# Optimization experiments

Measured on AMD Instinct MI355X. Metric: run time of the kernel, lower is better.

Reference implementation:

```python
import jax, jax.numpy as jnp
import numpy as np

N_SAMPLES = 32768
WINDOW = 512
STEP = WINDOW // 2            # 256
N_FRAMES = N_SAMPLES // STEP  # 128
N_COEFFS = WINDOW // 2 + 1    # 257
CPD = 16
N_RES = 32
EXPR = 4
BASE_RES = 0.5
CTRL_FRAMES = N_SAMPLES // 256  # 128 control frames, step=256


def fft_convolve(a, b):
    # zero-pad to 2N, multiply spectra, keep first N samples (matching repo's fft_convolve)
    n = max(a.shape[-1], b.shape[-1])
    fa = jnp.fft.rfft(a, n=2 * n, axis=-1)
    fb = jnp.fft.rfft(b, n=2 * n, axis=-1)
    out = jnp.fft.irfft(fa * fb, n=2 * n, axis=-1)
    return out[..., :n]


def upsample_with_holes(x, n_samples):
    # insert zeros between samples: out[..., ::step] = x
    lead, frames = x.shape[:-1], x.shape[-1]
    step = n_samples // frames
    out = jnp.zeros(lead + (frames, step), x.dtype)
    out = out.at[..., 0].set(x)
    return out.reshape(lead + (n_samples,))


def interpolate_last_axis(x, out_size):
    # linear interpolation along last axis (F.interpolate mode='linear', align_corners=False)
    in_size = x.shape[-1]
    scale = in_size / out_size
    pos = (jnp.arange(out_size, dtype=x.dtype) + 0.5) * scale - 0.5
    pos = jnp.clip(pos, 0.0, in_size - 1)
    lo = jnp.floor(pos).astype(jnp.int32)
    hi = jnp.minimum(lo + 1, in_size - 1)
    w = (pos - lo.astype(x.dtype))
    return x[..., lo] * (1.0 - w) + x[..., hi] * w


def materialize_resonances(amp, phase, decay):
    # amp/phase/decay: (R, C, E) -> (R, E, C)
    amp = jnp.transpose(amp, (0, 2, 1))
    phase = jnp.transpose(phase, (0, 2, 1))
    decay = jnp.transpose(decay, (0, 2, 1))
    d = BASE_RES + jax.nn.sigmoid(decay) * (1.0 - BASE_RES) * 0.9   # per-frame decay in (0.5, 0.95)
    start_phase = jnp.tanh(phase) * np.pi
    start_mags = jnp.abs(amp)
    # log-space scan of exponentially decaying spectral magnitudes: mags[t] = start * d^(t+1)
    t = jnp.arange(1, N_FRAMES + 1, dtype=amp.dtype)                  # (T,)
    log_mags = jnp.log(start_mags + 1e-12)[..., None, :] + t[:, None] * jnp.log(d)[..., None, :]
    spec = jnp.exp(log_mags) * jnp.exp(1j * start_phase[..., None, :])  # (R,E,T,C)
    frames = jnp.fft.irfft(spec, n=WINDOW, axis=-1)                     # (R,E,T,W)
    # overlap-add with hop STEP (W = 2*STEP): split halves, scatter into (T+1) slots
    first, second = frames[..., :STEP], frames[..., STEP:]
    out = jnp.zeros(frames.shape[:-2] + (N_FRAMES + 1, STEP), frames.dtype)
    out = out.at[..., :N_FRAMES, :].add(first)
    out = out.at[..., 1:, :].add(second)
    out = out.reshape(frames.shape[:-2] + ((N_FRAMES + 1) * STEP,))[..., :N_SAMPLES]
    return out.reshape(1, 1, N_RES, EXPR, N_SAMPLES)


def setup_inputs() -> dict:
    key = jax.random.key(0)
    ks = jax.random.split(key, 8)
    control_signal = jax.random.normal(ks[0], (2, 4, CPD, CTRL_FRAMES), dtype=jnp.float32)
    deformations = jax.random.normal(ks[1], (2, 4, EXPR, CTRL_FRAMES), dtype=jnp.float32)
    router = jax.random.uniform(ks[2], (CPD, N_RES), minval=-1.0, maxval=1.0, dtype=jnp.float32)
    gains = jax.random.uniform(ks[3], (N_RES, 1), minval=0.01, maxval=1.1, dtype=jnp.float32)
    amp = jax.random.uniform(ks[4], (N_RES, N_COEFFS, EXPR), minval=0.01, maxval=1.0, dtype=jnp.float32)
    phase = jax.random.uniform(ks[5], (N_RES, N_COEFFS, EXPR), minval=0.01, maxval=1.0, dtype=jnp.float32)
    decay = jax.random.uniform(ks[6], (N_RES, N_COEFFS, EXPR), minval=0.01, maxval=1.0, dtype=jnp.float32)
    impulse_noise = jax.random.uniform(ks[7], (128,), minval=-1.0, maxval=1.0, dtype=jnp.float32)
    return dict(control_signal=control_signal, deformations=deformations, router=router,
                gains=gains, amp=amp, phase=phase, decay=decay, impulse_noise=impulse_noise)


def reference(control_signal, deformations, router, gains, amp, phase, decay, impulse_noise):
    res = materialize_resonances(amp, phase, decay)            # (1,1,R,E,S)
    res = res / (jnp.linalg.norm(res, axis=-1, keepdims=True) + 1e-8)  # unit_norm

    B, NE, C, F = control_signal.shape
    routed = jnp.einsum('bncf,cr->bnrf', control_signal, router)  # (B,NE,R,F)
    before_upsample = routed

    routed = upsample_with_holes(routed[:, :, :, None, :], N_SAMPLES)  # (B,NE,R,1,S)

    n = jnp.arange(128, dtype=jnp.float32)
    hamming = 0.54 - 0.46 * jnp.cos(2.0 * jnp.pi * n / 128.0)  # torch periodic hamming
    impulse = hamming * impulse_noise
    impulse = jnp.pad(impulse, (0, N_SAMPLES - 128)).reshape(1, 1, 1, 1, N_SAMPLES)

    routed = fft_convolve(impulse, routed)
    conv = fft_convolve(routed, res)                           # (B,NE,R,E,S)

    base = jnp.zeros_like(deformations).at[:, :, 0:1, :].set(1.0)
    d = jax.nn.softmax(base + deformations, axis=-2)           # (B,NE,E,F)
    d = interpolate_last_axis(d[:, :, None, :, :], N_SAMPLES)  # (B,NE,1,E,S)

    x = jnp.sum(d * conv, axis=-2)                             # (B,NE,R,S)
    summed = jnp.tanh(x * jnp.abs(gains).reshape(1, 1, N_RES, 1))
    summed = jnp.sum(summed, axis=-2, keepdims=True)           # (B,NE,1,S)
    return summed, before_upsample
```

## Files before the change

kernel.cpp:

```cpp
#include <hip/hip_runtime.h>
#include <hip/hip_bf16.h>
#include <math.h>

#define N_SAMPLES 32768
#define STEP 256
#define N_FRAMES 128
#define N_COEFFS 257
#define KT 576
#define NKS 18
#define CPD 16
#define N_RES 32
#define EXPR 4
#define CTRL 128
#define NBN 8
#define BSTR 40
#define PI_F 3.14159265358979323846f

typedef __attribute__((ext_vector_type(8))) short bf16x8;
typedef __attribute__((ext_vector_type(4))) float f32x4;

__device__ __forceinline__ unsigned short f2bf(float x) {
    __hip_bfloat16 h = __float2bfloat16(x);
    return *(unsigned short*)&h;
}

__device__ __forceinline__ float bf2f(short u) {
    return __bfloat162float(*(__hip_bfloat16*)&u);
}

__device__ __forceinline__ float ftanh(float x) {
    float e = exp2f(x * 2.885390081777927f);
    return 1.0f - 2.0f * __builtin_amdgcn_rcpf(e + 1.0f);
}

__global__ __launch_bounds__(256) void k1m(const float* __restrict__ amp,
                                           const float* __restrict__ phase,
                                           const float* __restrict__ decay,
                                           float* __restrict__ res_raw,
                                           float* __restrict__ normp,
                                           float* __restrict__ out_zero) {
    __shared__ __align__(16) short Bs[2][64 * BSTR];
    __shared__ __align__(16) short Pb[KT];
    __shared__ __align__(16) short Zb[KT];
    __shared__ __align__(16) float Lf[KT];
    __shared__ __align__(16) float costab[512];
    __shared__ float red[256];
    int tid = threadIdx.x;
    int l = tid & 63, w = tid >> 6;
    int bid = blockIdx.x;
    out_zero[(size_t)bid * 256 + tid] = 0.f;
    int x = bid & 7, m = bid >> 3;
    int re = x * 16 + (m >> 3);
    int sub = m & 7;
    int bx = sub >> 1, jb = sub & 1;
    int r = re >> 2, e = re & 3;

    for (int i = tid; i < 512; i += 256)
        costab[i] = cosf((float)i * (2.0f * PI_F / 512.0f));

    for (int k = tid; k < KT; k += 256) {
        int kk = (k < 288) ? k : k - 288;
        float P = 0.f, Z = 0.f, L2v = 0.f;
        if (kk < N_COEFFS) {
            int src = (r * N_COEFFS + kk) * EXPR + e;
            float mm = fabsf(amp[src]) + 1e-12f;
            float ph = tanhf(phase[src]) * PI_F;
            float sg = 1.0f / (1.0f + expf(-decay[src]));
            float d  = 0.5f + 0.45f * sg;
            float wk = (kk == 0 || kk == 256) ? (1.0f / 512.0f) : (2.0f / 512.0f);
            float c  = (k < 288) ? (wk * mm * cosf(ph)) : (-wk * mm * sinf(ph));
            float sgn = (kk & 1) ? -1.f : 1.f;
            P = c * (d + sgn);
            Z = c * d;
            L2v = log2f(d);
        }
        int kloc = k & 31, blk = k >> 5;
        int p = blk * 32 + ((kloc >> 2) & 3) * 8 + ((kloc >> 4) & 1) * 4 + (kloc & 3);
        Pb[p] = (short)f2bf(P);
        Zb[p] = (short)f2bf(Z);
        Lf[p] = L2v;
    }
    __syncthreads();

    int o = (bx * 4 + w) * 16 + (l & 15);
    int g4v = l >> 4;
    float cb[8], sb[8], cc[8], sc[8];
    #pragma unroll
    for (int ee = 0; ee < 8; ++ee) {
        int delta = ((ee >> 2) << 4) + (g4v << 2) + (ee & 3);
        int xx = (delta * o) & 511;
        cb[ee] = costab[xx];
        sb[ee] = costab[(xx + 384) & 511];
        cc[ee] = cb[ee]; sc[ee] = sb[ee];
    }
    float rc, rs;
    {
        int xr = (32 * o) & 511;
        rc = costab[xr];
        rs = costab[(xr + 384) & 511];
    }

    int gj = tid >> 2;
    int gg = tid & 3;
    int jf = jb * 64 + gj;
    float jf_f = (float)jf;

    f32x4 acc[4] = {{0.f,0.f,0.f,0.f},{0.f,0.f,0.f,0.f},{0.f,0.f,0.f,0.f},{0.f,0.f,0.f,0.f}};
    int rrow = l & 15;
    int rcol = (l >> 4) * 8;

    auto GEN = [&](int s, int buf) {
        int kbp = s * 32 + gg * 8;
        bf16x8 vv;
        if (jf == 0) {
            vv = *(const bf16x8*)&Zb[kbp];
        } else {
            bf16x8 Pp = *(const bf16x8*)&Pb[kbp];
            f32x4 l0 = *(const f32x4*)&Lf[kbp];
            f32x4 l1 = *(const f32x4*)&Lf[kbp + 4];
            #pragma unroll
            for (int q = 0; q < 4; ++q) {
                vv[q]     = (short)f2bf(bf2f(Pp[q])     * exp2f(jf_f * l0[q]));
                vv[4 + q] = (short)f2bf(bf2f(Pp[4 + q]) * exp2f(jf_f * l1[q]));
            }
        }
        *(bf16x8*)&Bs[buf][gj * BSTR + gg * 8] = vv;
    };

    GEN(0, 0);
    __syncthreads();
    #pragma unroll
    for (int s = 0; s < NKS; ++s) {
        if (s < NKS - 1) GEN(s + 1, (s + 1) & 1);
        if (s == 9) {
            #pragma unroll
            for (int ee = 0; ee < 8; ++ee) { cc[ee] = cb[ee]; sc[ee] = sb[ee]; }
        }
        bf16x8 af;
        #pragma unroll
        for (int ee = 0; ee < 8; ++ee)
            af[ee] = (short)f2bf((s < 9) ? cc[ee] : sc[ee]);
        if (s != 8 && s != NKS - 1) {
            #pragma unroll
            for (int ee = 0; ee < 8; ++ee) {
                float t = cc[ee] * rc - sc[ee] * rs;
                sc[ee] = fmaf(cc[ee], rs, sc[ee] * rc);
                cc[ee] = t;
            }
        }
        const short* bp = &Bs[s & 1][0];
        #pragma unroll
        for (int jt = 0; jt < 4; ++jt) {
            bf16x8 bf = *(const bf16x8*)(bp + (jt * 16 + rrow) * BSTR + rcol);
            acc[jt] = __builtin_amdgcn_mfma_f32_16x16x32_bf16(af, bf, acc[jt], 0, 0, 0);
        }
        __syncthreads();
    }

    int otile = bx * 4 + w;
    int o0 = otile * 16 + ((l >> 4) & 3) * 4;
    int jbase = jb * 64 + (l & 15);
    float s2 = 0.f;
    #pragma unroll
    for (int jt = 0; jt < 4; ++jt) {
        int j = jbase + jt * 16;
        float4 v = make_float4(acc[jt][0], acc[jt][1], acc[jt][2], acc[jt][3]);
        s2 += v.x * v.x + v.y * v.y + v.z * v.z + v.w * v.w;
        *(float4*)&res_raw[(size_t)re * N_SAMPLES + j * STEP + o0] = v;
    }
    red[tid] = s2;
    __syncthreads();
    for (int st = 128; st > 0; st >>= 1) {
        if (tid < st) red[tid] += red[tid + st];
        __syncthreads();
    }
    if (tid == 0) normp[re * 8 + bx * 2 + jb] = red[0];
}

__global__ __launch_bounds__(256) void k3_impconv(const float* __restrict__ res_raw,
                                                  const float* __restrict__ normp,
                                                  const float* __restrict__ noise,
                                                  const float* __restrict__ control,
                                                  const float* __restrict__ router,
                                                  float* __restrict__ out_w,
                                                  uint4* __restrict__ Gbf_q) {
    __shared__ __align__(16) float st[8320];
    __shared__ __align__(16) float imp[128];
    int bid = blockIdx.x;
    int tid = threadIdx.x;
    if (bid >= 512) {
        int idx = (bid - 512) * 256 + tid;
        int f  = idx % CTRL;
        int r  = (idx / CTRL) % N_RES;
        int bn = idx / (CTRL * N_RES);
        float s = 0.f;
        #pragma unroll
        for (int c = 0; c < CPD; ++c)
            s += control[(bn * CPD + c) * CTRL + f] * router[c * N_RES + r];
        out_w[idx] = s;
        return;
    }
    int r  = (bid & 7) * 4 + ((bid >> 3) & 3);
    int t2 = bid >> 5;
    int e  = t2 & 3;
    int kt = t2 >> 2;
    int re = r * 4 + e;
    float ns = 0.f;
    #pragma unroll
    for (int i = 0; i < 8; ++i) ns += normp[re * 8 + i];
    float inv = 1.0f / (sqrtf(ns) + 1e-8f);
    if (tid < 128)
        imp[tid] = (0.54f - 0.46f * cosf((2.0f * PI_F / 128.0f) * (float)tid)) * noise[tid];
    const float* rp = res_raw + (size_t)re * N_SAMPLES;
    int gbase = kt * 8192 - 127;
    for (int i = tid; i < 8320; i += 256) {
        int g = gbase + i;
        st[i] = (g >= 0 && g < N_SAMPLES) ? rp[g] * inv : 0.f;
    }
    __syncthreads();

    int jg = tid >> 6;
    int o0 = (tid & 63) * 4;
    int jl[8];
    #pragma unroll
    for (int hh = 0; hh < 4; ++hh) {
        int h = jg * 4 + hh;
        int j0 = ((h >> 1) & 1) * 16 + (h >> 2) * 4 + (h & 1) * 2;
        jl[2 * hh] = j0;
        jl[2 * hh + 1] = j0 + 1;
    }
    float4 cur[8];
    float acc[8][4] = {};
    #pragma unroll
    for (int w = 0; w < 8; ++w)
        cur[w] = *(const float4*)&st[jl[w] * 256 + o0];

    for (int v = 0; v < 128; v += 4) {
        float4 im = *(const float4*)&imp[124 - v];
        float wt[4] = {im.w, im.z, im.y, im.x};
        #pragma unroll
        for (int w = 0; w < 8; ++w) {
            float4 nx = *(const float4*)&st[jl[w] * 256 + o0 + v + 4];
            float win[8] = {cur[w].x, cur[w].y, cur[w].z, cur[w].w, nx.x, nx.y, nx.z, nx.w};
            #pragma unroll
            for (int k = 0; k < 4; ++k)
                #pragma unroll
                for (int d = 0; d < 4; ++d)
                    acc[w][d] = fmaf(wt[k], win[d + k], acc[w][d]);
            cur[w] = nx;
        }
    }

    size_t rowb = (((size_t)(r * 4 + e) * 4 + kt) * 256 + o0) * 4;
    #pragma unroll
    for (int d = 0; d < 4; ++d) {
        uint4 outv;
        outv.x = (unsigned int)f2bf(acc[0][d]) | ((unsigned int)f2bf(acc[1][d]) << 16);
        outv.y = (unsigned int)f2bf(acc[2][d]) | ((unsigned int)f2bf(acc[3][d]) << 16);
        outv.z = (unsigned int)f2bf(acc[4][d]) | ((unsigned int)f2bf(acc[5][d]) << 16);
        outv.w = (unsigned int)f2bf(acc[6][d]) | ((unsigned int)f2bf(acc[7][d]) << 16);
        Gbf_q[rowb + (size_t)d * 4 + jg] = outv;
    }
}

__global__ __launch_bounds__(256) void k5m(const short* __restrict__ Gbf,
                                           const float* __restrict__ control,
                                           const float* __restrict__ router,
                                           const float* __restrict__ defo,
                                           const float* __restrict__ gains,
                                           float* __restrict__ out) {
    const int mt_of[20] = {0,1,2,2,3,3,4,4,4,5,5,5,6,6,6,6,7,7,7,7};
    const int kt_of[20] = {0,0,0,1,0,1,0,1,2,0,1,2,0,1,2,3,0,1,2,3};
    __shared__ __align__(16) float tab[130][4];
    __shared__ __align__(16) float wrow[4][128];
    __shared__ __align__(16) float part[4 * 64 * 33];
    int tid = threadIdx.x;
    int bid = blockIdx.x;
    int xcd = bid & 7;
    int on  = (bid >> 3) & 15;
    int bn  = bid >> 7;
    int l = tid & 63, w = tid >> 6;
    int r = xcd * 4 + w;
    float ga = fabsf(gains[r]);

    #pragma unroll
    for (int h = 0; h < 2; ++h) {
        int f = h * 64 + l;
        float s = 0.f;
        #pragma unroll
        for (int c2 = 0; c2 < CPD; ++c2)
            s += control[(bn * CPD + c2) * CTRL + f] * router[c2 * N_RES + r];
        wrow[w][f] = s;
    }
    if (tid < 130) {
        int f = tid - 1; f = f < 0 ? 0 : (f > 127 ? 127 : f);
        float v[EXPR]; float mx = -1e30f;
        #pragma unroll
        for (int e = 0; e < EXPR; ++e) {
            float xv = defo[(bn * EXPR + e) * CTRL + f] + (e == 0 ? 1.0f : 0.0f);
            v[e] = xv; mx = fmaxf(mx, xv);
        }
        float sum = 0.f;
        #pragma unroll
        for (int e = 0; e < EXPR; ++e) { v[e] = expf(v[e] - mx); sum += v[e]; }
        float is = 1.0f / sum;
        #pragma unroll
        for (int e = 0; e < EXPR; ++e) tab[tid][e] = v[e] * is;
    }
    __syncthreads();

    int n = l & 15, g4 = l >> 4;
    int ocol = on * 16 + n;
    int cofs = (on < 8) ? -1 : 0;
    float wg = (((float)ocol + 0.5f) * (1.0f / 256.0f) - 0.5f) - (float)cofs;

    bf16x8 wfrag[8];
    #pragma unroll
    for (int b = 0; b < 8; ++b) {
        bf16x8 v;
        #pragma unroll
        for (int ee = 0; ee < 8; ++ee) {
            int diff = b * 16 + n - ((ee >> 2) << 4) - (g4 << 2) - (ee & 3);
            float val = (diff >= 0) ? wrow[w][diff] : 0.f;
            v[ee] = (short)f2bf(val);
        }
        wfrag[b] = v;
    }

    const short* gb = Gbf + ((size_t)r * 16) * (256 * 32);
    float xsum[8][4] = {};
    #pragma unroll
    for (int eh = 0; eh < 2; ++eh) {
        bf16x8 bfr[2][4];
        #pragma unroll
        for (int ei = 0; ei < 2; ++ei)
            #pragma unroll
            for (int kt = 0; kt < 4; ++kt) {
                int ekt = (eh * 2 + ei) * 4 + kt;
                bfr[ei][kt] = *(const bf16x8*)(gb + ((size_t)ekt * 256 + ocol) * 32 + g4 * 8);
            }
        f32x4 acc[2][8] = {};
        #pragma unroll
        for (int pr = 0; pr < 20; ++pr) {
            int mt = mt_of[pr], kt = kt_of[pr];
            int b = mt - 2 * kt;
            acc[0][mt] = __builtin_amdgcn_mfma_f32_16x16x32_bf16(wfrag[b], bfr[0][kt], acc[0][mt], 0, 0, 0);
            acc[1][mt] = __builtin_amdgcn_mfma_f32_16x16x32_bf16(wfrag[b], bfr[1][kt], acc[1][mt], 0, 0, 0);
        }
        #pragma unroll
        for (int mt = 0; mt < 8; ++mt) {
            int base = mt * 16 + (g4 << 2) + cofs + 1;
            f32x4 tv[5];
            #pragma unroll
            for (int q = 0; q < 5; ++q)
                tv[q] = *(const f32x4*)&tab[base + q][0];
            #pragma unroll
            for (int q = 0; q < 4; ++q) {
                #pragma unroll
                for (int ei = 0; ei < 2; ++ei) {
                    int e = eh * 2 + ei;
                    float de = fmaf(wg, tv[q + 1][e] - tv[q][e], tv[q][e]);
                    xsum[mt][q] = fmaf(de, acc[ei][mt][q], xsum[mt][q]);
                }
            }
        }
    }

    float* myp = &part[(w * 64 + l) * 33];
    #pragma unroll
    for (int mt = 0; mt < 8; ++mt)
        #pragma unroll
        for (int q = 0; q < 4; ++q)
            myp[mt * 4 + q] = ftanh(xsum[mt][q] * ga);
    __syncthreads();

    int rn = tid & 15, jgr = tid >> 4;
    float* ob = out + (size_t)bn * N_SAMPLES + on * 16 + rn;
    #pragma unroll
    for (int jj = 0; jj < 8; ++jj) {
        int j = jgr * 8 + jj;
        int mt = j >> 4, rem = j & 15;
        int gg4 = rem >> 2, q = rem & 3;
        int ll = gg4 * 16 + rn;
        int idx = mt * 4 + q;
        float s = part[ll * 33 + idx]
                + part[(64 + ll) * 33 + idx]
                + part[(128 + ll) * 33 + idx]
                + part[(192 + ll) * 33 + idx];
        atomicAdd(ob + j * STEP, s);
    }
}

extern "C" void kernel_launch(void* const* d_in, const int* in_sizes, int n_in,
                              void* d_out, int out_size, void* d_ws, size_t ws_size,
                              hipStream_t stream) {
    const float* control = (const float*)d_in[0];
    const float* defo    = (const float*)d_in[1];
    const float* router  = (const float*)d_in[2];
    const float* gains   = (const float*)d_in[3];
    const float* amp     = (const float*)d_in[4];
    const float* phase   = (const float*)d_in[5];
    const float* decay   = (const float*)d_in[6];
    const float* noise   = (const float*)d_in[7];

    float* out_summed = (float*)d_out;
    float* out_w      = (float*)d_out + NBN * N_SAMPLES;

    char* ws = (char*)d_ws;
    short* Gbf = (short*)ws;
    float* normp = (float*)(ws + 8388608);
    float* res_raw = (float*)(ws + 16777216);

    k1m<<<1024, 256, 0, stream>>>(amp, phase, decay, res_raw, normp, out_summed);
    k3_impconv<<<640, 256, 0, stream>>>(res_raw, normp, noise, control, router, out_w, (uint4*)Gbf);
    k5m<<<1024, 256, 0, stream>>>(Gbf, control, router, defo, gains, out_summed);
}
```

Before: 71.37 us.

## Store intermediate resonances as bf16 and compute all expressions' MFMAs at once

Measured after the change: 71.82 us. Within noise of the previous version (+0.6%).

```diff
diff --git a/kernel.cpp b/kernel.cpp
--- a/kernel.cpp
+++ b/kernel.cpp
@@ -36,7 +36,7 @@
 __global__ __launch_bounds__(256) void k1m(const float* __restrict__ amp,
                                            const float* __restrict__ phase,
                                            const float* __restrict__ decay,
-                                           float* __restrict__ res_raw,
+                                           short* __restrict__ res_bf,
                                            float* __restrict__ normp,
                                            float* __restrict__ out_zero) {
     __shared__ __align__(16) short Bs[2][64 * BSTR];
@@ -164,9 +164,12 @@
     #pragma unroll
     for (int jt = 0; jt < 4; ++jt) {
         int j = jbase + jt * 16;
-        float4 v = make_float4(acc[jt][0], acc[jt][1], acc[jt][2], acc[jt][3]);
-        s2 += v.x * v.x + v.y * v.y + v.z * v.z + v.w * v.w;
-        *(float4*)&res_raw[(size_t)re * N_SAMPLES + j * STEP + o0] = v;
+        f32x4 v = acc[jt];
+        s2 += v[0] * v[0] + v[1] * v[1] + v[2] * v[2] + v[3] * v[3];
+        uint2 pk;
+        pk.x = (unsigned int)f2bf(v[0]) | ((unsigned int)f2bf(v[1]) << 16);
+        pk.y = (unsigned int)f2bf(v[2]) | ((unsigned int)f2bf(v[3]) << 16);
+        *(uint2*)&res_bf[(size_t)re * N_SAMPLES + j * STEP + o0] = pk;
     }
     red[tid] = s2;
     __syncthreads();
@@ -177,7 +180,7 @@
     if (tid == 0) normp[re * 8 + bx * 2 + jb] = red[0];
 }
 
-__global__ __launch_bounds__(256) void k3_impconv(const float* __restrict__ res_raw,
+__global__ __launch_bounds__(256) void k3_impconv(const short* __restrict__ res_bf,
                                                   const float* __restrict__ normp,
                                                   const float* __restrict__ noise,
                                                   const float* __restrict__ control,
@@ -211,11 +214,11 @@
     float inv = 1.0f / (sqrtf(ns) + 1e-8f);
     if (tid < 128)
         imp[tid] = (0.54f - 0.46f * cosf((2.0f * PI_F / 128.0f) * (float)tid)) * noise[tid];
-    const float* rp = res_raw + (size_t)re * N_SAMPLES;
+    const short* rp = res_bf + (size_t)re * N_SAMPLES;
     int gbase = kt * 8192 - 127;
     for (int i = tid; i < 8320; i += 256) {
         int g = gbase + i;
-        st[i] = (g >= 0 && g < N_SAMPLES) ? rp[g] * inv : 0.f;
+        st[i] = (g >= 0 && g < N_SAMPLES) ? bf2f(rp[g]) * inv : 0.f;
     }
     __syncthreads();
 
@@ -328,50 +331,42 @@
     }
 
     const short* gb = Gbf + ((size_t)r * 16) * (256 * 32);
-    float xsum[8][4] = {};
-    #pragma unroll
-    for (int eh = 0; eh < 2; ++eh) {
-        bf16x8 bfr[2][4];
-        #pragma unroll
-        for (int ei = 0; ei < 2; ++ei)
+    bf16x8 bfr[4][4];
+    #pragma unroll
+    for (int e = 0; e < 4; ++e)
+        #pragma unroll
+        for (int kt = 0; kt < 4; ++kt)
+            bfr[e][kt] = *(const bf16x8*)(gb + ((size_t)(e * 4 + kt) * 256 + ocol) * 32 + g4 * 8);
+
+    f32x4 acc[4][8] = {};
+    #pragma unroll
+    for (int pr = 0; pr < 20; ++pr) {
+        int mt = mt_of[pr], kt = kt_of[pr];
+        int b = mt - 2 * kt;
+        #pragma unroll
+        for (int e = 0; e < 4; ++e)
+            acc[e][mt] = __builtin_amdgcn_mfma_f32_16x16x32_bf16(wfrag[b], bfr[e][kt], acc[e][mt], 0, 0, 0);
+    }
+
+    float* myp = &part[(w * 64 + l) * 33];
+    #pragma unroll
+    for (int mt = 0; mt < 8; ++mt) {
+        int base = mt * 16 + (g4 << 2) + cofs + 1;
+        f32x4 tv[5];
+        #pragma unroll
+        for (int q = 0; q < 5; ++q)
+            tv[q] = *(const f32x4*)&tab[base + q][0];
+        #pragma unroll
+        for (int q = 0; q < 4; ++q) {
+            float xv = 0.f;
             #pragma unroll
-            for (int kt = 0; kt < 4; ++kt) {
-                int ekt = (eh * 2 + ei) * 4 + kt;
-                bfr[ei][kt] = *(const bf16x8*)(gb + ((size_t)ekt * 256 + ocol) * 32 + g4 * 8);
+            for (int e = 0; e < 4; ++e) {
+                float de = fmaf(wg, tv[q + 1][e] - tv[q][e], tv[q][e]);
+                xv = fmaf(de, acc[e][mt][q], xv);
             }
-        f32x4 acc[2][8] = {};
-        #pragma unroll
-        for (int pr = 0; pr < 20; ++pr) {
-            int mt = mt_of[pr], kt = kt_of[pr];
-            int b = mt - 2 * kt;
-            acc[0][mt] = __builtin_amdgcn_mfma_f32_16x16x32_bf16(wfrag[b], bfr[0][kt], acc[0][mt], 0, 0, 0);
-            acc[1][mt] = __builtin_amdgcn_mfma_f32_16x16x32_bf16(wfrag[b], bfr[1][kt], acc[1][mt], 0, 0, 0);
-        }
-        #pragma unroll
-        for (int mt = 0; mt < 8; ++mt) {
-            int base = mt * 16 + (g4 << 2) + cofs + 1;
-            f32x4 tv[5];
-            #pragma unroll
-            for (int q = 0; q < 5; ++q)
-                tv[q] = *(const f32x4*)&tab[base + q][0];
-            #pragma unroll
-            for (int q = 0; q < 4; ++q) {
-                #pragma unroll
-                for (int ei = 0; ei < 2; ++ei) {
-                    int e = eh * 2 + ei;
-                    float de = fmaf(wg, tv[q + 1][e] - tv[q][e], tv[q][e]);
-                    xsum[mt][q] = fmaf(de, acc[ei][mt][q], xsum[mt][q]);
-                }
-            }
-        }
-    }
-
-    float* myp = &part[(w * 64 + l) * 33];
-    #pragma unroll
-    for (int mt = 0; mt < 8; ++mt)
-        #pragma unroll
-        for (int q = 0; q < 4; ++q)
-            myp[mt * 4 + q] = ftanh(xsum[mt][q] * ga);
+            myp[mt * 4 + q] = ftanh(xv * ga);
+        }
+    }
     __syncthreads();
 
     int rn = tid & 15, jgr = tid >> 4;
@@ -409,9 +404,9 @@
     char* ws = (char*)d_ws;
     short* Gbf = (short*)ws;
     float* normp = (float*)(ws + 8388608);
-    float* res_raw = (float*)(ws + 16777216);
-
-    k1m<<<1024, 256, 0, stream>>>(amp, phase, decay, res_raw, normp, out_summed);
-    k3_impconv<<<640, 256, 0, stream>>>(res_raw, normp, noise, control, router, out_w, (uint4*)Gbf);
+    short* res_bf = (short*)(ws + 16777216);
+
+    k1m<<<1024, 256, 0, stream>>>(amp, phase, decay, res_bf, normp, out_summed);
+    k3_impconv<<<640, 256, 0, stream>>>(res_bf, normp, noise, control, router, out_w, (uint4*)Gbf);
     k5m<<<1024, 256, 0, stream>>>(Gbf, control, router, defo, gains, out_summed);
 }
```
